# Kernel optimization log

Measured on AMD Instinct MI355X. Metric: run time of the kernel, lower is better.

The kernel has to match this reference:

```python
import jax, jax.numpy as jnp
import numpy as np

B, A, D = 2048, 256, 8
FA, FB, FP = 64, 16, 256


def setup_inputs() -> dict:
    key = jax.random.key(0)
    k1, k2, k3, k4, k5 = jax.random.split(key, 5)
    atoms = jax.random.normal(k1, (B, A, FA), dtype=jnp.float32)
    bonds = jax.random.normal(k2, (B, A, D, FB), dtype=jnp.float32)
    # edges use -1 as padding for missing neighbors
    edges = jax.random.randint(k3, (B, A, D), -1, A, dtype=jnp.int32)
    fan_in = FA + FB
    limit = np.sqrt(6.0 / (fan_in + FP)).astype(np.float32)  # glorot_uniform
    W = jax.random.uniform(k4, (fan_in, FP), minval=-limit, maxval=limit, dtype=jnp.float32)
    b = jnp.zeros((FP,), dtype=jnp.float32)
    return {"atoms": atoms, "bonds": bonds, "edges": edges, "W": W, "b": b}


def reference(atoms, bonds, edges, W, b):
    # atom degree from edge list (-1 = padded neighbor slot)
    atom_degrees = jnp.sum((edges != -1).astype(jnp.float32), axis=-1, keepdims=True)  # [B,A,1]
    general_atom_mask = (atom_degrees != 0).astype(atoms.dtype)                        # [B,A,1]
    summed_bond_features = jnp.sum(bonds, axis=-2)                                     # [B,A,FB]
    atoms_bonds = jnp.concatenate([atoms, summed_bond_features], axis=-1)              # [B,A,FA+FB]
    # TimeDistributed Dense with relu, applied per atom
    fp_unmasked = jax.nn.relu(jnp.einsum('baf,fo->bao', atoms_bonds, W) + b)           # [B,A,FP]
    fp_masked = fp_unmasked * general_atom_mask
    return jnp.sum(fp_masked, axis=-2)                                                 # [B,FP]
```

## Files before the change

### kernel.cpp

```cpp
#include <hip/hip_runtime.h>


#define NB 2048
#define NA 256
#define ND 8
#define NFA 64
#define NFB 16
#define NF 80
#define NFP 256
#define PITCH 96

typedef __attribute__((ext_vector_type(8))) short short8;
typedef __attribute__((ext_vector_type(4))) float f32x4;

static __device__ __forceinline__ unsigned short f2bf(float f) {
    unsigned int u = __float_as_uint(f);
    return (unsigned short)((u + 0x7FFFu + ((u >> 16) & 1u)) >> 16);
}

__launch_bounds__(256, 3)
__global__ void ngf_mfma_kernel(const float4* __restrict__ atoms4,
                                const float4* __restrict__ bonds4,
                                const int4*   __restrict__ edges4,
                                const float*  __restrict__ W,
                                const float*  __restrict__ bias,
                                float* __restrict__ out)
{
    const int b    = blockIdx.x;
    const int tid  = threadIdx.x;
    const int wave = tid >> 6;
    const int lane = tid & 63;
    const int lrow = lane & 15;
    const int lgrp = lane >> 4;

    __shared__ unsigned short X[NA * PITCH];
    __shared__ float maskf[NA];

    const size_t molAtom = (size_t)b * NA;

    short8 bf[3][4];
    float  bia[4];
    #pragma unroll
    for (int nt = 0; nt < 4; ++nt) {
        const int c = (wave * 4 + nt) * 16 + lrow;
        bia[nt] = bias[c];
        #pragma unroll
        for (int ks = 0; ks < 3; ++ks) {
            short8 v;
            #pragma unroll
            for (int j = 0; j < 8; ++j) {
                const int k = ks * 32 + lgrp * 8 + j;
                float w = (k < NF) ? W[k * NFP + c] : 0.0f;
                v[j] = (short)f2bf(w);
            }
            bf[ks][nt] = v;
        }
    }

    #pragma unroll 4
    for (int it = 0; it < 16; ++it) {
        const int flat = it * 256 + tid;
        const int a = flat >> 4, k4 = flat & 15;
        float4 v = atoms4[(molAtom + a) * 16 + k4];
        ushort4 o;
        o.x = f2bf(v.x); o.y = f2bf(v.y); o.z = f2bf(v.z); o.w = f2bf(v.w);
        *(ushort4*)&X[a * PITCH + k4 * 4] = o;
    }
    #pragma unroll
    for (int p = 0; p < 4; ++p) {
        const int a = p * 64 + (tid >> 2);
        const int q = tid & 3;
        const float4* bp = bonds4 + (molAtom + a) * 32 + q;
        float4 s = {0.0f, 0.0f, 0.0f, 0.0f};
        #pragma unroll
        for (int d = 0; d < 8; ++d) {
            float4 v = bp[d * 4];
            s.x += v.x; s.y += v.y; s.z += v.z; s.w += v.w;
        }
        ushort4 o;
        o.x = f2bf(s.x); o.y = f2bf(s.y); o.z = f2bf(s.z); o.w = f2bf(s.w);
        *(ushort4*)&X[a * PITCH + NFA + q * 4] = o;
    }
    {
        const int a = tid;
        int4 e0 = edges4[(molAtom + a) * 2];
        int4 e1 = edges4[(molAtom + a) * 2 + 1];
        bool any = (e0.x != -1) | (e0.y != -1) | (e0.z != -1) | (e0.w != -1)
                 | (e1.x != -1) | (e1.y != -1) | (e1.z != -1) | (e1.w != -1);
        maskf[a] = any ? 1.0f : 0.0f;
        uint4 z = {0u, 0u, 0u, 0u};
        *(uint4*)&X[a * PITCH + 80] = z;
        *(uint4*)&X[a * PITCH + 88] = z;
    }
    __syncthreads();

    float colsum[4] = {0.0f, 0.0f, 0.0f, 0.0f};
    for (int s = 0; s < 16; ++s) {
        const int row = s * 16 + lrow;
        const unsigned short* xr = &X[row * PITCH + lgrp * 8];
        short8 a0 = *(const short8*)(xr);
        short8 a1 = *(const short8*)(xr + 32);
        short8 a2 = *(const short8*)(xr + 64);
        float4 m4 = *(const float4*)&maskf[s * 16 + lgrp * 4];
        #pragma unroll
        for (int nt = 0; nt < 4; ++nt) {
            f32x4 acc = {0.0f, 0.0f, 0.0f, 0.0f};
            acc = __builtin_amdgcn_mfma_f32_16x16x32_bf16(a0, bf[0][nt], acc, 0, 0, 0);
            acc = __builtin_amdgcn_mfma_f32_16x16x32_bf16(a1, bf[1][nt], acc, 0, 0, 0);
            acc = __builtin_amdgcn_mfma_f32_16x16x32_bf16(a2, bf[2][nt], acc, 0, 0, 0);
            const float bv = bia[nt];
            colsum[nt] += fmaxf(acc[0] + bv, 0.0f) * m4.x
                        + fmaxf(acc[1] + bv, 0.0f) * m4.y
                        + fmaxf(acc[2] + bv, 0.0f) * m4.z
                        + fmaxf(acc[3] + bv, 0.0f) * m4.w;
        }
    }

    #pragma unroll
    for (int nt = 0; nt < 4; ++nt) {
        float v = colsum[nt];
        v += __shfl_xor(v, 16, 64);
        v += __shfl_xor(v, 32, 64);
        if (lane < 16)
            out[(size_t)b * NFP + (wave * 4 + nt) * 16 + lane] = v;
    }
}

extern "C" void kernel_launch(void* const* d_in, const int* in_sizes, int n_in,
                              void* d_out, int out_size, void* d_ws, size_t ws_size,
                              hipStream_t stream) {
    const float4* atoms4 = (const float4*)d_in[0];
    const float4* bonds4 = (const float4*)d_in[1];
    const int4*   edges4 = (const int4*)d_in[2];
    const float*  W      = (const float*)d_in[3];
    const float*  bias   = (const float*)d_in[4];
    float* out = (float*)d_out;

    ngf_mfma_kernel<<<NB, 256, 0, stream>>>(atoms4, bonds4, edges4, W, bias, out);
}
```

Baseline: 102.6 us.

## Split each molecule across two blocks, prepack W fragments, add reduction kernel

A one-off prep kernel converts W into bf16 MFMA B-fragments in the workspace, so each block loads ready-made fragments instead of converting W itself. The main kernel now handles 128 atoms per block, giving twice as many blocks with half the LDS, and raises launch_bounds occupancy from 3 to 4. The aim is better latency hiding on this bandwidth-bound streaming load. A third kernel sums the two per-half partial results. The cost is two extra launches and a partial-sum buffer. LDS pitch also changes to 100, which leaves 16-byte vector LDS accesses misaligned on odd rows and may split them or cost extra.

```diff
diff --git a/kernel.cpp b/kernel.cpp
--- a/kernel.cpp
+++ b/kernel.cpp
@@ -8,7 +8,11 @@
 #define NFB 16
 #define NF 80
 #define NFP 256
-#define PITCH 96
+#define PITCH 100
+#define AH 128
+
+#define WFRAG_BYTES (16 * 3 * 64 * 16)
+#define PART_OFF    (64 * 1024)
 
 typedef __attribute__((ext_vector_type(8))) short short8;
 typedef __attribute__((ext_vector_type(4))) float f32x4;
@@ -18,59 +22,68 @@
     return (unsigned short)((u + 0x7FFFu + ((u >> 16) & 1u)) >> 16);
 }
 
-__launch_bounds__(256, 3)
+__global__ void ngf_prep_w(const float* __restrict__ W, short8* __restrict__ wfrag)
+{
+    const int gid  = blockIdx.x;
+    const int nt   = gid / 3;
+    const int ks   = gid % 3;
+    const int lane = threadIdx.x;
+    const int c    = nt * 16 + (lane & 15);
+    short8 v;
+    #pragma unroll
+    for (int j = 0; j < 8; ++j) {
+        const int k = ks * 32 + (lane >> 4) * 8 + j;
+        float w = (k < NF) ? W[k * NFP + c] : 0.0f;
+        v[j] = (short)f2bf(w);
+    }
+    wfrag[gid * 64 + lane] = v;
+}
+
+__launch_bounds__(256, 4)
 __global__ void ngf_mfma_kernel(const float4* __restrict__ atoms4,
                                 const float4* __restrict__ bonds4,
                                 const int4*   __restrict__ edges4,
-                                const float*  __restrict__ W,
+                                const short8* __restrict__ wfrag,
                                 const float*  __restrict__ bias,
-                                float* __restrict__ out)
+                                float* __restrict__ part)
 {
-    const int b    = blockIdx.x;
+    const int bid  = blockIdx.x;
     const int tid  = threadIdx.x;
     const int wave = tid >> 6;
     const int lane = tid & 63;
     const int lrow = lane & 15;
     const int lgrp = lane >> 4;
 
-    __shared__ unsigned short X[NA * PITCH];
-    __shared__ float maskf[NA];
+    __shared__ unsigned short X[AH * PITCH];
+    __shared__ float maskf[AH];
 
-    const size_t molAtom = (size_t)b * NA;
+    const size_t atomBase = (size_t)bid * AH;
 
     short8 bf[3][4];
     float  bia[4];
     #pragma unroll
     for (int nt = 0; nt < 4; ++nt) {
-        const int c = (wave * 4 + nt) * 16 + lrow;
-        bia[nt] = bias[c];
+        const int ntg = wave * 4 + nt;
+        bia[nt] = bias[ntg * 16 + lrow];
         #pragma unroll
-        for (int ks = 0; ks < 3; ++ks) {
-            short8 v;
-            #pragma unroll
-            for (int j = 0; j < 8; ++j) {
-                const int k = ks * 32 + lgrp * 8 + j;
-                float w = (k < NF) ? W[k * NFP + c] : 0.0f;
-                v[j] = (short)f2bf(w);
-            }
-            bf[ks][nt] = v;
-        }
+        for (int ks = 0; ks < 3; ++ks)
+            bf[ks][nt] = wfrag[(ntg * 3 + ks) * 64 + lane];
     }
 
-    #pragma unroll 4
-    for (int it = 0; it < 16; ++it) {
+    #pragma unroll
+    for (int it = 0; it < 8; ++it) {
         const int flat = it * 256 + tid;
         const int a = flat >> 4, k4 = flat & 15;
-        float4 v = atoms4[(molAtom + a) * 16 + k4];
+        float4 v = atoms4[(atomBase + a) * 16 + k4];
         ushort4 o;
         o.x = f2bf(v.x); o.y = f2bf(v.y); o.z = f2bf(v.z); o.w = f2bf(v.w);
         *(ushort4*)&X[a * PITCH + k4 * 4] = o;
     }
     #pragma unroll
-    for (int p = 0; p < 4; ++p) {
+    for (int p = 0; p < 2; ++p) {
         const int a = p * 64 + (tid >> 2);
         const int q = tid & 3;
-        const float4* bp = bonds4 + (molAtom + a) * 32 + q;
+        const float4* bp = bonds4 + (atomBase + a) * 32 + q;
         float4 s = {0.0f, 0.0f, 0.0f, 0.0f};
         #pragma unroll
         for (int d = 0; d < 8; ++d) {
@@ -81,10 +94,10 @@
         o.x = f2bf(s.x); o.y = f2bf(s.y); o.z = f2bf(s.z); o.w = f2bf(s.w);
         *(ushort4*)&X[a * PITCH + NFA + q * 4] = o;
     }
-    {
+    if (tid < AH) {
         const int a = tid;
-        int4 e0 = edges4[(molAtom + a) * 2];
-        int4 e1 = edges4[(molAtom + a) * 2 + 1];
+        int4 e0 = edges4[(atomBase + a) * 2];
+        int4 e1 = edges4[(atomBase + a) * 2 + 1];
         bool any = (e0.x != -1) | (e0.y != -1) | (e0.z != -1) | (e0.w != -1)
                  | (e1.x != -1) | (e1.y != -1) | (e1.z != -1) | (e1.w != -1);
         maskf[a] = any ? 1.0f : 0.0f;
@@ -95,7 +108,8 @@
     __syncthreads();
 
     float colsum[4] = {0.0f, 0.0f, 0.0f, 0.0f};
-    for (int s = 0; s < 16; ++s) {
+    #pragma unroll 2
+    for (int s = 0; s < 8; ++s) {
         const int row = s * 16 + lrow;
         const unsigned short* xr = &X[row * PITCH + lgrp * 8];
         short8 a0 = *(const short8*)(xr);
@@ -122,8 +136,16 @@
         v += __shfl_xor(v, 16, 64);
         v += __shfl_xor(v, 32, 64);
         if (lane < 16)
-            out[(size_t)b * NFP + (wave * 4 + nt) * 16 + lane] = v;
+            part[(size_t)bid * NFP + (wave * 4 + nt) * 16 + lane] = v;
     }
+}
+
+__global__ void ngf_reduce(const float* __restrict__ part, float* __restrict__ out)
+{
+    const int g   = blockIdx.x * 256 + threadIdx.x;
+    const int mol = g >> 8;
+    const int col = g & 255;
+    out[g] = part[(size_t)(2 * mol) * NFP + col] + part[(size_t)(2 * mol + 1) * NFP + col];
 }
 
 extern "C" void kernel_launch(void* const* d_in, const int* in_sizes, int n_in,
@@ -136,5 +158,10 @@
     const float*  bias   = (const float*)d_in[4];
     float* out = (float*)d_out;
 
-    ngf_mfma_kernel<<<NB, 256, 0, stream>>>(atoms4, bonds4, edges4, W, bias, out);
+    short8* wfrag = (short8*)d_ws;
+    float*  part  = (float*)((char*)d_ws + PART_OFF);
+
+    ngf_prep_w<<<48, 64, 0, stream>>>(W, wfrag);
+    ngf_mfma_kernel<<<NB * 2, 256, 0, stream>>>(atoms4, bonds4, edges4, wfrag, bias, part);
+    ngf_reduce<<<2048, 256, 0, stream>>>(part, out);
 }
```

Result: faster. 89.63 us (-12.6%).
